# Kernel optimization log

Hardware: AMD Instinct MI355X
Metric: run time of the kernel (lower is better)

## Reference

```python
import jax, jax.numpy as jnp
import numpy as np

DIM = 96
NUM_EXPERTS = 4
TOP_K = 1

def setup_inputs() -> dict:
    key = jax.random.key(0)
    ks = jax.random.split(key, 8)
    B, C, H, W = 16, DIM, 128, 128
    E = NUM_EXPERTS
    x = jax.random.normal(ks[0], (B, C, H, W), dtype=jnp.float32)
    # per-expert depthwise 3x3 conv (groups=C): torch weight [C,1,3,3]
    dw_w = jax.random.normal(ks[1], (E, C, 1, 3, 3), dtype=jnp.float32) * 0.1
    dw_b = jax.random.normal(ks[2], (E, C), dtype=jnp.float32) * 0.05
    # per-expert pointwise 1x1 conv: torch weight [C,C,1,1]
    pw_w = jax.random.normal(ks[3], (E, C, C, 1, 1), dtype=jnp.float32) * 0.1
    pw_b = jax.random.normal(ks[4], (E, C), dtype=jnp.float32) * 0.05
    # router linear: torch weight [E, C]
    router_w = jax.random.normal(ks[5], (E, C), dtype=jnp.float32) * 0.1
    router_b = jax.random.normal(ks[6], (E,), dtype=jnp.float32) * 0.05
    return {"x": x, "dw_w": dw_w, "dw_b": dw_b, "pw_w": pw_w, "pw_b": pw_b,
            "router_w": router_w, "router_b": router_b}

def _conv(x, w, groups):
    return jax.lax.conv_general_dilated(
        x, w, window_strides=(1, 1), padding='SAME',
        dimension_numbers=('NCHW', 'OIHW', 'NCHW'),
        feature_group_count=groups)

def _expert(x, dw_w, dw_b, pw_w, pw_b):
    C = x.shape[1]
    h = _conv(x, dw_w, groups=C) + dw_b[None, :, None, None]   # depthwise 3x3
    h = jax.nn.gelu(h, approximate=False)                       # torch GELU (erf)
    return _conv(h, pw_w, groups=1) + pw_b[None, :, None, None] # 1x1 conv

def reference(x, dw_w, dw_b, pw_w, pw_b, router_w, router_b):
    B, C, H, W = x.shape
    E = dw_w.shape[0]
    # router: global avg pool -> linear -> softmax
    pooled = jnp.mean(x, axis=(2, 3))                            # [B, C]
    logits = pooled @ router_w.T + router_b                      # [B, E]
    router_weights = jax.nn.softmax(logits, axis=-1)
    top_weights, top_indices = jax.lax.top_k(router_weights, TOP_K)  # [B, k]
    top_weights = top_weights / (jnp.sum(top_weights, axis=-1, keepdims=True) + 1e-8)
    # run all experts (faithful to the original, which does not dispatch)
    expert_outputs = jnp.stack(
        [_expert(x, dw_w[e], dw_b[e], pw_w[e], pw_b[e]) for e in range(E)],
        axis=1)                                                  # [B, E, C, H, W]
    # scatter top-k weights into dense gates [B, E]
    gates = jnp.zeros((B, E), dtype=x.dtype)
    gates = gates.at[jnp.arange(B)[:, None], top_indices].set(top_weights)
    return jnp.einsum('bechw,be->bchw', expert_outputs, gates)
```

## Files before the change

kernel.cpp:

```cpp
#include <hip/hip_runtime.h>
#include <math.h>

#define DIM 96
#define NE 4
#define HH 128
#define WW 128
#define BB 16
#define KP 24
#define HSROW (KP * 2)
#define HSBUF (WW * HSROW)

typedef __attribute__((ext_vector_type(8))) __bf16 bf16x8;
typedef __attribute__((ext_vector_type(4))) float floatx4;

__device__ __forceinline__ unsigned short f2bf(float f) {
    unsigned u = __builtin_bit_cast(unsigned, f);
    unsigned r = u + 0x7FFFu + ((u >> 16) & 1u);
    return (unsigned short)(r >> 16);
}
__device__ __forceinline__ unsigned pack2(float a, float b) {
    return (unsigned)f2bf(a) | ((unsigned)f2bf(b) << 16);
}

__device__ __forceinline__ float dpp_up1(float v) {
    return __builtin_bit_cast(float, __builtin_amdgcn_mov_dpp(
        __builtin_bit_cast(int, v), 0x138, 0xF, 0xF, true));
}
__device__ __forceinline__ float dpp_down1(float v) {
    return __builtin_bit_cast(float, __builtin_amdgcn_mov_dpp(
        __builtin_bit_cast(int, v), 0x130, 0xF, 0xF, true));
}

__device__ __forceinline__ void barrier_lds_only() {
    asm volatile("s_waitcnt lgkmcnt(0)" ::: "memory");
    __builtin_amdgcn_s_barrier();
}

__device__ __forceinline__ float gelu_erf(float h) {
    const float x = h * 0.70710678118654752f;
    const float a = fabsf(x);
    const float t = __builtin_amdgcn_rcpf(__builtin_fmaf(0.3275911f, a, 1.0f));
    float p = __builtin_fmaf(1.061405429f, t, -1.453152027f);
    p = __builtin_fmaf(p, t, 1.421413741f);
    p = __builtin_fmaf(p, t, -0.284496736f);
    p = __builtin_fmaf(p, t, 0.254829592f);
    p *= t;
    const float e = __expf(-x * x);
    float erfv = __builtin_fmaf(-p, e, 1.0f);
    erfv = copysignf(erfv, x);
    return 0.5f * h * (1.0f + erfv);
}

__global__ __launch_bounds__(256) void pool_kernel(const float* __restrict__ x,
                                                   float* __restrict__ pooled) {
    const int bc = blockIdx.x;
    const float4* p = (const float4*)(x + (size_t)bc * (HH * WW));
    const int t = threadIdx.x;
    float s = 0.f;
#pragma unroll
    for (int k = 0; k < (HH * WW / 4) / 256; ++k) {
        float4 v = p[t + k * 256];
        s += v.x + v.y + v.z + v.w;
    }
#pragma unroll
    for (int off = 32; off; off >>= 1) s += __shfl_down(s, off, 64);
    __shared__ float ls[4];
    if ((t & 63) == 0) ls[t >> 6] = s;
    __syncthreads();
    if (t == 0) pooled[bc] = (ls[0] + ls[1] + ls[2] + ls[3]) * (1.0f / (HH * WW));
}

__device__ __forceinline__ void issue_sub(const float* __restrict__ x, int b,
                                          int cbase, int cg, int rr0, int r,
                                          int rr2, int p4, float4 f[2][3]) {
#pragma unroll
    for (int u = 0; u < 2; ++u) {
        const float* pl = x + (size_t)(b * DIM + cbase + cg * 2 + u) * (HH * WW);
        f[u][0] = *(const float4*)(pl + rr0 * WW + p4);
        f[u][1] = *(const float4*)(pl + r   * WW + p4);
        f[u][2] = *(const float4*)(pl + rr2 * WW + p4);
    }
}

__device__ __forceinline__ void compute_sub(const float4 f[2][3],
                                            const float (*dwc)[12], int cb,
                                            int cg, float lmask, float rmask,
                                            unsigned char* hsbuf, int p4,
                                            unsigned swz) {
    float hq[2][4];
#pragma unroll
    for (int u = 0; u < 2; ++u) {
        const int c = cb + cg * 2 + u;
        const float4 wA = *(const float4*)&dwc[c][0];
        const float4 wB = *(const float4*)&dwc[c][4];
        const float4 wC = *(const float4*)&dwc[c][8];
        float h0 = wC.y, h1 = wC.y, h2 = wC.y, h3 = wC.y;
#pragma unroll
        for (int row = 0; row < 3; ++row) {
            const float ta = (row == 0) ? wA.x : ((row == 1) ? wA.w : wB.z);
            const float tb = (row == 0) ? wA.y : ((row == 1) ? wB.x : wB.w);
            const float tc = (row == 0) ? wA.z : ((row == 1) ? wB.y : wC.x);
            const float4 f4 = f[u][row];
            const float vl = dpp_up1(f4.w) * lmask;
            const float vr = dpp_down1(f4.x) * rmask;
            h0 = __builtin_fmaf(ta, vl,   __builtin_fmaf(tb, f4.x, __builtin_fmaf(tc, f4.y, h0)));
            h1 = __builtin_fmaf(ta, f4.x, __builtin_fmaf(tb, f4.y, __builtin_fmaf(tc, f4.z, h1)));
            h2 = __builtin_fmaf(ta, f4.y, __builtin_fmaf(tb, f4.z, __builtin_fmaf(tc, f4.w, h2)));
            h3 = __builtin_fmaf(ta, f4.z, __builtin_fmaf(tb, f4.w, __builtin_fmaf(tc, vr, h3)));
        }
        hq[u][0] = gelu_erf(h0);
        hq[u][1] = gelu_erf(h1);
        hq[u][2] = gelu_erf(h2);
        hq[u][3] = gelu_erf(h3);
    }
    const unsigned wb0 = (unsigned)(p4 * HSROW + cg * 4);
#pragma unroll
    for (int j = 0; j < 4; ++j) {
        const unsigned off = (wb0 + (unsigned)j * HSROW) ^ swz;
        *(unsigned*)(hsbuf + off) = pack2(hq[0][j], hq[1][j]);
    }
}

__global__ __launch_bounds__(256, 3) void moe_main(
    const float* __restrict__ x, const float* __restrict__ dw_w,
    const float* __restrict__ dw_b, const float* __restrict__ pw_w,
    const float* __restrict__ pw_b, const float* __restrict__ pooled,
    const float* __restrict__ rw, const float* __restrict__ rb,
    float* __restrict__ out) {
    __shared__ __align__(16) unsigned char hsb[4 * HSBUF];
    __shared__ float dwc[DIM][12];
    __shared__ float lsm[4];

    const int t = threadIdx.x;
    const unsigned bid = blockIdx.x;
    const int xcd = bid & 7;
    const int s = bid >> 3;
    const int b = xcd * 2 + (s >> 7);
    const int r = s & 127;

    const int lane = t & 63, w = t >> 6;
    const int wm = w & 1, wn = w >> 1;
    const int ln = lane & 15, kg = lane >> 4;
    const int cobase = wm * 48, pxbase = wn * 64;

    const int g32 = t & 31;
    const int p4 = g32 * 4;
    const int cg = t >> 5;
    const unsigned swz = (unsigned)((g32 & 7) << 4);
    const float lmask = (p4 == 0) ? 0.f : 1.f;
    const float rmask = (p4 == 124) ? 0.f : 1.f;

    const float m0 = (r > 0) ? 1.f : 0.f;
    const float m2 = (r < HH - 1) ? 1.f : 0.f;
    const int rr0 = (r > 0) ? r - 1 : 0;
    const int rr2 = (r < HH - 1) ? r + 1 : HH - 1;

    float4 fA[2][3], fB[2][3];
    issue_sub(x, b, 0, cg, rr0, r, rr2, p4, fA);
    issue_sub(x, b, 16, cg, rr0, r, rr2, p4, fB);

    {
        float part = pooled[b * DIM + lane] * rw[w * DIM + lane];
        if (lane < 32)
            part += pooled[b * DIM + 64 + lane] * rw[w * DIM + 64 + lane];
#pragma unroll
        for (int off = 32; off; off >>= 1) part += __shfl_down(part, off, 64);
        if (lane == 0) lsm[w] = part + rb[w];
    }
    barrier_lds_only();
    int e;
    float g;
    {
        const float l0 = lsm[0], l1 = lsm[1], l2 = lsm[2], l3 = lsm[3];
        float m = l0; int mi = 0;
        if (l1 > m) { m = l1; mi = 1; }
        if (l2 > m) { m = l2; mi = 2; }
        if (l3 > m) { m = l3; mi = 3; }
        const float denom = __expf(l0 - m) + __expf(l1 - m) +
                            __expf(l2 - m) + __expf(l3 - m);
        const float wv = 1.0f / denom;
        g = wv / (wv + 1e-8f);
        e = mi;
    }

    for (int j = t; j < DIM * 12; j += 256) {
        const int c = j / 12, q = j - c * 12;
        float v = 0.f;
        if (q < 9) {
            v = dw_w[((size_t)e * DIM + c) * 9 + q];
            if (q < 3) v *= m0;
            if (q >= 6) v *= m2;
        } else if (q == 9) v = dw_b[e * DIM + c];
        dwc[c][q] = v;
    }
    barrier_lds_only();

    floatx4 acc[3][4];
#pragma unroll
    for (int i = 0; i < 3; ++i)
#pragma unroll
        for (int j = 0; j < 4; ++j) acc[i][j] = (floatx4){0.f, 0.f, 0.f, 0.f};

#pragma unroll
    for (int pair = 0; pair < 3; ++pair) {
        const int cb = pair * 32;
        unsigned char* h0 = hsb + (unsigned)((pair & 1) * 2) * HSBUF;
        unsigned char* h1 = h0 + HSBUF;
        float4 a0[3], a1[3];
#pragma unroll
        for (int mf = 0; mf < 3; ++mf) {
            const float* ap = pw_w + ((size_t)e * DIM + cobase + mf * 16 + ln) * DIM
                              + cb + kg * 8;
            a0[mf] = *(const float4*)ap;
            a1[mf] = *(const float4*)(ap + 4);
        }
        compute_sub(fA, dwc, cb, cg, lmask, rmask, h0, p4, swz);
        if (pair < 2) issue_sub(x, b, cb + 32, cg, rr0, r, rr2, p4, fA);
        bf16x8 af[3];
#pragma unroll
        for (int mf = 0; mf < 3; ++mf) {
            uint4 u;
            u.x = pack2(a0[mf].x, a0[mf].y);
            u.y = pack2(a0[mf].z, a0[mf].w);
            u.z = pack2(a1[mf].x, a1[mf].y);
            u.w = pack2(a1[mf].z, a1[mf].w);
            af[mf] = __builtin_bit_cast(bf16x8, u);
        }
        compute_sub(fB, dwc, cb + 16, cg, lmask, rmask, h1, p4, swz);
        if (pair < 2) issue_sub(x, b, cb + 48, cg, rr0, r, rr2, p4, fB);
        barrier_lds_only();

        const unsigned qbase = (unsigned)((pair & 1) * 2 + (kg >> 1)) * HSBUF;
        bf16x8 bfr[4];
#pragma unroll
        for (int nf = 0; nf < 4; ++nf) {
            const int pxv = pxbase + nf * 16 + ln;
            const unsigned boff = (unsigned)((pxv * HSROW + (kg & 1) * 16) ^
                                             (((pxv >> 2) & 7) << 4));
            bfr[nf] = *(const bf16x8*)(hsb + qbase + boff);
        }
#pragma unroll
        for (int mf = 0; mf < 3; ++mf)
#pragma unroll
            for (int nf = 0; nf < 4; ++nf)
                acc[mf][nf] = __builtin_amdgcn_mfma_f32_16x16x32_bf16(
                    af[mf], bfr[nf], acc[mf][nf], 0, 0, 0);
    }

#pragma unroll
    for (int mf = 0; mf < 3; ++mf) {
#pragma unroll
        for (int rr = 0; rr < 4; ++rr) {
            const int co = cobase + mf * 16 + kg * 4 + rr;
            const float bias = pw_b[e * DIM + co];
            float* orow = out + ((size_t)(b * DIM + co) * HH + r) * WW;
#pragma unroll
            for (int nf = 0; nf < 4; ++nf)
                orow[pxbase + nf * 16 + ln] = (acc[mf][nf][rr] + bias) * g;
        }
    }
}

extern "C" void kernel_launch(void* const* d_in, const int* in_sizes, int n_in,
                              void* d_out, int out_size, void* d_ws, size_t ws_size,
                              hipStream_t stream) {
    const float* x    = (const float*)d_in[0];
    const float* dw_w = (const float*)d_in[1];
    const float* dw_b = (const float*)d_in[2];
    const float* pw_w = (const float*)d_in[3];
    const float* pw_b = (const float*)d_in[4];
    const float* rw   = (const float*)d_in[5];
    const float* rb   = (const float*)d_in[6];
    float* out = (float*)d_out;

    float* pooled = (float*)d_ws;

    pool_kernel<<<BB * DIM, 256, 0, stream>>>(x, pooled);
    moe_main<<<HH * BB, 256, 0, stream>>>(x, dw_w, dw_b, pw_w, pw_b,
                                          pooled, rw, rb, out);
}
```

Measured before the change: 67.35 us.

## Process two image rows per 512-thread block instead of one row per 256-thread block

Each block now covers two output rows with 512 threads and 8 waves, so the pixel (N) dimension of the pointwise MFMA doubles to 256 per block. The vertical boundary masks move from the LDS weight table into per-thread multipliers, because the two rows in a block can have different edge conditions. The aim is to amortise the per-block router, weight staging and pw_w fragment loads over twice as many pixels. In exchange the LDS footprint doubles and the occupancy target drops to 2 blocks per CU.

```diff
diff --git a/kernel.cpp b/kernel.cpp
--- a/kernel.cpp
+++ b/kernel.cpp
@@ -8,7 +8,7 @@
 #define BB 16
 #define KP 24
 #define HSROW (KP * 2)
-#define HSBUF (WW * HSROW)
+#define HSBUF (256 * HSROW)
 
 typedef __attribute__((ext_vector_type(8))) __bf16 bf16x8;
 typedef __attribute__((ext_vector_type(4))) float floatx4;
@@ -72,19 +72,20 @@
 
 __device__ __forceinline__ void issue_sub(const float* __restrict__ x, int b,
                                           int cbase, int cg, int rr0, int r,
-                                          int rr2, int p4, float4 f[2][3]) {
+                                          int rr2, int pin, float4 f[2][3]) {
 #pragma unroll
     for (int u = 0; u < 2; ++u) {
         const float* pl = x + (size_t)(b * DIM + cbase + cg * 2 + u) * (HH * WW);
-        f[u][0] = *(const float4*)(pl + rr0 * WW + p4);
-        f[u][1] = *(const float4*)(pl + r   * WW + p4);
-        f[u][2] = *(const float4*)(pl + rr2 * WW + p4);
+        f[u][0] = *(const float4*)(pl + rr0 * WW + pin);
+        f[u][1] = *(const float4*)(pl + r   * WW + pin);
+        f[u][2] = *(const float4*)(pl + rr2 * WW + pin);
     }
 }
 
 __device__ __forceinline__ void compute_sub(const float4 f[2][3],
                                             const float (*dwc)[12], int cb,
                                             int cg, float lmask, float rmask,
+                                            float mTop, float mBot,
                                             unsigned char* hsbuf, int p4,
                                             unsigned swz) {
     float hq[2][4];
@@ -97,9 +98,10 @@
         float h0 = wC.y, h1 = wC.y, h2 = wC.y, h3 = wC.y;
 #pragma unroll
         for (int row = 0; row < 3; ++row) {
-            const float ta = (row == 0) ? wA.x : ((row == 1) ? wA.w : wB.z);
-            const float tb = (row == 0) ? wA.y : ((row == 1) ? wB.x : wB.w);
-            const float tc = (row == 0) ? wA.z : ((row == 1) ? wB.y : wC.x);
+            const float rm = (row == 0) ? mTop : ((row == 2) ? mBot : 1.0f);
+            const float ta = ((row == 0) ? wA.x : ((row == 1) ? wA.w : wB.z)) * rm;
+            const float tb = ((row == 0) ? wA.y : ((row == 1) ? wB.x : wB.w)) * rm;
+            const float tc = ((row == 0) ? wA.z : ((row == 1) ? wB.y : wC.x)) * rm;
             const float4 f4 = f[u][row];
             const float vl = dpp_up1(f4.w) * lmask;
             const float vr = dpp_down1(f4.x) * rmask;
@@ -121,7 +123,7 @@
     }
 }
 
-__global__ __launch_bounds__(256, 3) void moe_main(
+__global__ __launch_bounds__(512, 2) void moe_main(
     const float* __restrict__ x, const float* __restrict__ dw_w,
     const float* __restrict__ dw_b, const float* __restrict__ pw_w,
     const float* __restrict__ pw_b, const float* __restrict__ pooled,
@@ -135,31 +137,33 @@
     const unsigned bid = blockIdx.x;
     const int xcd = bid & 7;
     const int s = bid >> 3;
-    const int b = xcd * 2 + (s >> 7);
-    const int r = s & 127;
+    const int b = xcd * 2 + (s >> 6);
+    const int r0 = (s & 63) * 2;
 
     const int lane = t & 63, w = t >> 6;
     const int wm = w & 1, wn = w >> 1;
     const int ln = lane & 15, kg = lane >> 4;
     const int cobase = wm * 48, pxbase = wn * 64;
 
-    const int g32 = t & 31;
-    const int p4 = g32 * 4;
-    const int cg = t >> 5;
-    const unsigned swz = (unsigned)((g32 & 7) << 4);
-    const float lmask = (p4 == 0) ? 0.f : 1.f;
-    const float rmask = (p4 == 124) ? 0.f : 1.f;
-
-    const float m0 = (r > 0) ? 1.f : 0.f;
-    const float m2 = (r < HH - 1) ? 1.f : 0.f;
-    const int rr0 = (r > 0) ? r - 1 : 0;
-    const int rr2 = (r < HH - 1) ? r + 1 : HH - 1;
+    const int g64 = t & 63;
+    const int p4 = g64 * 4;
+    const int cg = t >> 6;
+    const unsigned swz = (unsigned)((g64 & 7) << 4);
+    const int pin = p4 & 127;
+    const float lmask = (pin == 0) ? 0.f : 1.f;
+    const float rmask = (pin == 124) ? 0.f : 1.f;
+
+    const int myr = r0 + (p4 >> 7);
+    const float mTop = (myr > 0) ? 1.f : 0.f;
+    const float mBot = (myr < HH - 1) ? 1.f : 0.f;
+    const int rr0 = (myr > 0) ? myr - 1 : 0;
+    const int rr2 = (myr < HH - 1) ? myr + 1 : HH - 1;
 
     float4 fA[2][3], fB[2][3];
-    issue_sub(x, b, 0, cg, rr0, r, rr2, p4, fA);
-    issue_sub(x, b, 16, cg, rr0, r, rr2, p4, fB);
-
-    {
+    issue_sub(x, b, 0, cg, rr0, myr, rr2, pin, fA);
+    issue_sub(x, b, 16, cg, rr0, myr, rr2, pin, fB);
+
+    if (w < NE) {
         float part = pooled[b * DIM + lane] * rw[w * DIM + lane];
         if (lane < 32)
             part += pooled[b * DIM + 64 + lane] * rw[w * DIM + 64 + lane];
@@ -183,14 +187,11 @@
         e = mi;
     }
 
-    for (int j = t; j < DIM * 12; j += 256) {
+    for (int j = t; j < DIM * 12; j += 512) {
         const int c = j / 12, q = j - c * 12;
         float v = 0.f;
-        if (q < 9) {
-            v = dw_w[((size_t)e * DIM + c) * 9 + q];
-            if (q < 3) v *= m0;
-            if (q >= 6) v *= m2;
-        } else if (q == 9) v = dw_b[e * DIM + c];
+        if (q < 9) v = dw_w[((size_t)e * DIM + c) * 9 + q];
+        else if (q == 9) v = dw_b[e * DIM + c];
         dwc[c][q] = v;
     }
     barrier_lds_only();
@@ -214,8 +215,8 @@
             a0[mf] = *(const float4*)ap;
             a1[mf] = *(const float4*)(ap + 4);
         }
-        compute_sub(fA, dwc, cb, cg, lmask, rmask, h0, p4, swz);
-        if (pair < 2) issue_sub(x, b, cb + 32, cg, rr0, r, rr2, p4, fA);
+        compute_sub(fA, dwc, cb, cg, lmask, rmask, mTop, mBot, h0, p4, swz);
+        if (pair < 2) issue_sub(x, b, cb + 32, cg, rr0, myr, rr2, pin, fA);
         bf16x8 af[3];
 #pragma unroll
         for (int mf = 0; mf < 3; ++mf) {
@@ -226,8 +227,8 @@
             u.w = pack2(a1[mf].z, a1[mf].w);
             af[mf] = __builtin_bit_cast(bf16x8, u);
         }
-        compute_sub(fB, dwc, cb + 16, cg, lmask, rmask, h1, p4, swz);
-        if (pair < 2) issue_sub(x, b, cb + 48, cg, rr0, r, rr2, p4, fB);
+        compute_sub(fB, dwc, cb + 16, cg, lmask, rmask, mTop, mBot, h1, p4, swz);
+        if (pair < 2) issue_sub(x, b, cb + 48, cg, rr0, myr, rr2, pin, fB);
         barrier_lds_only();
 
         const unsigned qbase = (unsigned)((pair & 1) * 2 + (kg >> 1)) * HSBUF;
@@ -253,10 +254,12 @@
         for (int rr = 0; rr < 4; ++rr) {
             const int co = cobase + mf * 16 + kg * 4 + rr;
             const float bias = pw_b[e * DIM + co];
-            float* orow = out + ((size_t)(b * DIM + co) * HH + r) * WW;
-#pragma unroll
-            for (int nf = 0; nf < 4; ++nf)
-                orow[pxbase + nf * 16 + ln] = (acc[mf][nf][rr] + bias) * g;
+            float* obase = out + ((size_t)(b * DIM + co) * HH + r0) * WW;
+#pragma unroll
+            for (int nf = 0; nf < 4; ++nf) {
+                const int px = pxbase + nf * 16 + ln;
+                obase[(px >> 7) * WW + (px & 127)] = (acc[mf][nf][rr] + bias) * g;
+            }
         }
     }
 }
@@ -276,6 +279,6 @@
     float* pooled = (float*)d_ws;
 
     pool_kernel<<<BB * DIM, 256, 0, stream>>>(x, pooled);
-    moe_main<<<HH * BB, 256, 0, stream>>>(x, dw_w, dw_b, pw_w, pw_b,
-                                          pooled, rw, rb, out);
-}
+    moe_main<<<(HH / 2) * BB, 512, 0, stream>>>(x, dw_w, dw_b, pw_w, pw_b,
+                                                pooled, rw, rb, out);
+}
```

New measurement: 81.27 us. 1.21x slower.
